# Performance work log

Hardware: AMD Instinct MI355X
Metric: run time of the kernel (lower is better)

Reference implementation:

```python
import jax, jax.numpy as jnp
import numpy as np

BS, C_IN, NY, NX = 8, 256, 80, 80
C, NC, NA, N = 256, 80, 1, 16384
K = 3  # 3x3 sparse convs, padding 1


def setup_inputs() -> dict:
    key = jax.random.key(0)
    ks = jax.random.split(key, 16)
    w = lambda k, shape: jax.random.normal(k, shape, jnp.float32) * 0.02
    x = jax.random.normal(ks[0], (BS, C_IN, NY, NX), jnp.float32)
    bi = jax.random.randint(ks[1], (N,), 0, BS)
    yi = jax.random.randint(ks[2], (N,), 0, NY)
    xi = jax.random.randint(ks[3], (N,), 0, NX)
    indices = jnp.stack([bi, yi, xi], axis=1).astype(jnp.int64)
    return {
        'x': x,
        'indices': indices,
        'stem_w': w(ks[4], (C, C_IN)),        'stem_b': w(ks[5], (C,)),
        'cls_conv_w': w(ks[6], (C, C * K * K)), 'cls_conv_b': w(ks[7], (C,)),
        'reg_conv_w': w(ks[8], (C, C * K * K)), 'reg_conv_b': w(ks[9], (C,)),
        'cls_pred_w': w(ks[10], (NA * NC, C)),  'cls_pred_b': w(ks[11], (NA * NC,)),
        'reg_pred_w': w(ks[12], (NA * 4, C)),   'reg_pred_b': w(ks[13], (NA * 4,)),
        'obj_pred_w': w(ks[14], (NA * 1, C)),   'obj_pred_b': w(ks[15], (NA * 1,)),
    }


def _gather_patches(stem, indices):
    """Gather flattened KxK patches at (b,y,x) indices.

    Matches F.unfold ordering: flattened as [c, kh, kw].
    stem: [bs, c, ny, nx] -> returns [N, c*K*K].
    """
    pad = K // 2
    # NHWC padded feature map: [bs, ny+2p, nx+2p, c]
    padded = jnp.pad(stem.transpose(0, 2, 3, 1),
                     ((0, 0), (pad, pad), (pad, pad), (0, 0)))
    bi, yi, xi = indices[:, 0], indices[:, 1], indices[:, 2]
    d = jnp.arange(K)
    yy = yi[:, None, None] + d[None, :, None]   # [N, K, 1]
    xx = xi[:, None, None] + d[None, None, :]   # [N, 1, K]
    patches = padded[bi[:, None, None], yy, xx]  # [N, K, K, c]
    n = patches.shape[0]
    return patches.transpose(0, 3, 1, 2).reshape(n, -1)  # [N, c*K*K]


def reference(x, indices, stem_w, stem_b, cls_conv_w, cls_conv_b,
              reg_conv_w, reg_conv_b, cls_pred_w, cls_pred_b,
              reg_pred_w, reg_pred_b, obj_pred_w, obj_pred_b):
    # dense 1x1 stem conv + SiLU
    stem = jax.nn.silu(jnp.einsum('bchw,oc->bohw', x, stem_w)
                       + stem_b[None, :, None, None])
    # sparse 3x3 convs: gather patches -> linear -> SiLU
    pf = _gather_patches(stem, indices)                 # [N, C*9]
    cls_feat = jax.nn.silu(pf @ cls_conv_w.T + cls_conv_b)
    reg_feat = jax.nn.silu(pf @ reg_conv_w.T + reg_conv_b)
    n = pf.shape[0]
    cls = (cls_feat @ cls_pred_w.T + cls_pred_b).reshape(n, NA, NC)
    reg = (reg_feat @ reg_pred_w.T + reg_pred_b).reshape(n, NA, 4)
    obj = (reg_feat @ obj_pred_w.T + obj_pred_b).reshape(n, NA, 1)
    y_sp = jnp.concatenate([reg, obj, cls], axis=-1).reshape(n, NA * (5 + NC))
    return y_sp
```

## Files before the change

### kernel.cpp

```cpp
#include <hip/hip_runtime.h>

typedef unsigned short u16;
typedef __attribute__((ext_vector_type(4))) float f32x4;
typedef __attribute__((ext_vector_type(8))) short s16x8;

#define BM 128
#define BN 128
#define BK 32

__device__ inline float bf2f(u16 u) {
    unsigned v = ((unsigned)u) << 16;
    return __builtin_bit_cast(float, v);
}
__device__ inline u16 f2bf(float f) {
    unsigned u = __builtin_bit_cast(unsigned, f);
    unsigned r = (u + 0x7FFFu + ((u >> 16) & 1u)) >> 16;
    return (u16)r;
}

typedef const __attribute__((address_space(1))) void* gptr_t;
typedef __attribute__((address_space(3))) void* lptr_t;
__device__ inline void gload16(const u16* gp, u16* lp) {
    __builtin_amdgcn_global_load_lds((gptr_t)gp, (lptr_t)lp, 16, 0, 0);
}

__global__ __launch_bounds__(256) void fused_pre(
    const float* __restrict__ x, const int* __restrict__ idx,
    const float* __restrict__ stem_w,
    const float* __restrict__ cls_conv_w, const float* __restrict__ cls_conv_b,
    const float* __restrict__ reg_conv_w, const float* __restrict__ reg_conv_b,
    const float* __restrict__ cls_pred_w, const float* __restrict__ cls_pred_b,
    const float* __restrict__ reg_pred_w, const float* __restrict__ reg_pred_b,
    const float* __restrict__ obj_pred_w, const float* __restrict__ obj_pred_b,
    u16* __restrict__ xT, u16* __restrict__ Wsb, u16* __restrict__ Wc,
    u16* __restrict__ Wf, int* __restrict__ rowoff,
    float* __restrict__ bc, float* __restrict__ bp, u16* __restrict__ zpage) {
    __shared__ u16 tile[64 * 258];
    const int blk = blockIdx.x;
    const int t = threadIdx.x;

    if (blk < 800) {
        int b = blk / 100, hw0 = (blk % 100) * 64;
        int l = t & 63, w = t >> 6;
        const float* xb = x + (size_t)b * 256 * 6400 + hw0 + l;
#pragma unroll 4
        for (int k = 0; k < 64; ++k) {
            int c = w + k * 4;
            tile[l * 258 + c] = f2bf(xb[(size_t)c * 6400]);
        }
        __syncthreads();
        u16* outb = xT + ((size_t)b * 6400 + hw0) * 256;
#pragma unroll
        for (int i = 0; i < 8; ++i) {
            int hw = w * 16 + i * 2 + (l >> 5);
            int c = (l & 31) * 8;
            *(int4*)(outb + (size_t)hw * 256 + c) = *(const int4*)&tile[hw * 258 + c];
        }
    } else if (blk < 1312) {
        int o = blk - 800;
        const float* src = (o < 256) ? (cls_conv_w + (size_t)o * 2304)
                                     : (reg_conv_w + (size_t)(o - 256) * 2304);
        u16* dst = Wc + (size_t)o * 2304;
#pragma unroll
        for (int it = 0; it < 9; ++it) {
            int kk = it * 256 + t;
            int j = kk >> 8, c = kk & 255;
            dst[kk] = f2bf(src[c * 9 + j]);
        }
    } else if (blk < 1888) {
        int i = (blk - 1312) * 256 + t;
        int n = i / 9, j = i % 9;
        int b = idx[n * 3 + 0], y = idx[n * 3 + 1], xx0 = idx[n * 3 + 2];
        int yy = y + j / 3 - 1;
        int xx = xx0 + j % 3 - 1;
        rowoff[i] = ((unsigned)yy < 80u && (unsigned)xx < 80u)
                        ? (b * 6400 + yy * 80 + xx) * 256 : -1;
    } else if (blk < 1952) {
        int base = (blk - 1888) * 1024;
#pragma unroll
        for (int it = 0; it < 4; ++it) {
            int i = base + it * 256 + t;
            Wsb[i] = f2bf(stem_w[i]);
        }
    } else if (blk < 1984) {
        int base = (blk - 1952) * 2048;
#pragma unroll
        for (int it = 0; it < 8; ++it) {
            int i = base + it * 256 + t;
            int o = i >> 9, k = i & 511;
            float v = 0.f;
            if (o < 4)       { if (k >= 256) v = reg_pred_w[o * 256 + (k - 256)]; }
            else if (o == 4) { if (k >= 256) v = obj_pred_w[k - 256]; }
            else if (o < 85) { if (k < 256)  v = cls_pred_w[(o - 5) * 256 + k]; }
            Wf[i] = f2bf(v);
        }
    } else {
        for (int i = t; i < 512; i += 256)
            bc[i] = (i < 256) ? cls_conv_b[i] : reg_conv_b[i - 256];
        if (t < 128) {
            float v = 0.f;
            if (t < 4) v = reg_pred_b[t];
            else if (t == 4) v = obj_pred_b[0];
            else if (t < 85) v = cls_pred_b[t - 5];
            bp[t] = v;
        }
        zpage[t] = 0;
    }
}

template <int EPI>
__global__ __launch_bounds__(256, 2) void gemm_bt(
    const u16* __restrict__ A, const u16* __restrict__ B,
    const float* __restrict__ bias, void* __restrict__ Dv,
    int K, int ldd, int storeN) {
    __shared__ __align__(16) u16 lA[BM * BK];
    __shared__ __align__(16) u16 lB[BN * BK];
    const int tid = threadIdx.x;
    const int lane = tid & 63;
    const int wid = tid >> 6;
    const int wm = wid >> 1, wn = wid & 1;
    const int m0 = blockIdx.x * BM;
    const int n0 = blockIdx.y * BN;

    const int srow = lane >> 2;
    const int scol = (lane & 3) * 8;
    const int arow = lane & 15;
    const int khalf = (lane >> 4) * 8;

    f32x4 acc[4][4] = {};

    for (int k0 = 0; k0 < K; k0 += BK) {
#pragma unroll
        for (int r = 0; r < 2; ++r) {
            int row = r * 64 + wid * 16 + srow;
            gload16(A + (size_t)(m0 + row) * K + k0 + scol, lA + r * 2048 + wid * 512);
            gload16(B + (size_t)(n0 + row) * K + k0 + scol, lB + r * 2048 + wid * 512);
        }
        __syncthreads();
        s16x8 af[4], bfr[4];
#pragma unroll
        for (int f = 0; f < 4; ++f) {
            af[f]  = *(const s16x8*)&lA[(wm * 64 + f * 16 + arow) * BK + khalf];
            bfr[f] = *(const s16x8*)&lB[(wn * 64 + f * 16 + arow) * BK + khalf];
        }
#pragma unroll
        for (int i = 0; i < 4; ++i)
#pragma unroll
            for (int j = 0; j < 4; ++j)
                acc[i][j] = __builtin_amdgcn_mfma_f32_16x16x32_bf16(af[i], bfr[j],
                                                                    acc[i][j], 0, 0, 0);
        __syncthreads();
    }

#pragma unroll
    for (int i = 0; i < 4; ++i) {
        int gr0 = m0 + wm * 64 + i * 16 + (lane >> 4) * 4;
#pragma unroll
        for (int j = 0; j < 4; ++j) {
            int gc = n0 + wn * 64 + j * 16 + (lane & 15);
            if (EPI == 1 && gc >= storeN) continue;
            float bb = bias[gc];
#pragma unroll
            for (int r = 0; r < 4; ++r) {
                float v = acc[i][j][r] + bb;
                if (EPI == 0) {
                    v = v / (1.0f + __expf(-v));
                    ((u16*)Dv)[(size_t)(gr0 + r) * ldd + gc] = f2bf(v);
                } else {
                    ((float*)Dv)[(size_t)(gr0 + r) * ldd + gc] = v;
                }
            }
        }
    }
}

__global__ __launch_bounds__(256, 4) void gemm_conv(
    const u16* __restrict__ stem, const int* __restrict__ rowoff,
    const u16* __restrict__ zpage, const u16* __restrict__ B,
    const float* __restrict__ bias, u16* __restrict__ D) {
    __shared__ __align__(16) u16 lA[128 * 64];
    __shared__ __align__(16) u16 lB[64 * 64];
    const int tid = threadIdx.x;
    const int lane = tid & 63;
    const int wid = tid >> 6;
    const int wm = wid >> 1, wn = wid & 1;
    const int m0 = blockIdx.x * 128;
    const int n0 = blockIdx.y * 64;

    const int srw = lane >> 3;
    const int cc  = lane & 7;
    const int arow = lane & 15;
    const int khi  = lane >> 4;

    f32x4 acc[4][2] = {};

    for (int k0 = 0; k0 < 2304; k0 += 64) {
        const int j  = k0 >> 8;
        const int c0 = k0 & 255;
        const int gch = (cc ^ srw) * 8;
#pragma unroll
        for (int r = 0; r < 4; ++r) {
            int row = r * 32 + wid * 8 + srw;
            int roff = rowoff[(m0 + row) * 9 + j];
            const u16* srcA = (roff < 0) ? (zpage + gch)
                                         : (stem + roff + c0 + gch);
            gload16(srcA, lA + (r * 32 + wid * 8) * 64);
        }
#pragma unroll
        for (int r = 0; r < 2; ++r) {
            int row = r * 32 + wid * 8 + srw;
            gload16(B + (size_t)(n0 + row) * 2304 + k0 + gch,
                    lB + (r * 32 + wid * 8) * 64);
        }
        __syncthreads();
        s16x8 af[2][4], bfr[2][2];
        const int sa = arow & 7;
#pragma unroll
        for (int f = 0; f < 4; ++f) {
            int ra = (wm * 64 + f * 16 + arow) * 64;
#pragma unroll
            for (int ks = 0; ks < 2; ++ks) {
                int q = ks * 4 + khi;
                af[ks][f] = *(const s16x8*)&lA[ra + ((q ^ sa) << 3)];
            }
        }
#pragma unroll
        for (int jj = 0; jj < 2; ++jj) {
            int rb = (wn * 32 + jj * 16 + arow) * 64;
#pragma unroll
            for (int ks = 0; ks < 2; ++ks) {
                int q = ks * 4 + khi;
                bfr[ks][jj] = *(const s16x8*)&lB[rb + ((q ^ sa) << 3)];
            }
        }
#pragma unroll
        for (int ks = 0; ks < 2; ++ks)
#pragma unroll
            for (int i = 0; i < 4; ++i)
#pragma unroll
                for (int jj = 0; jj < 2; ++jj)
                    acc[i][jj] = __builtin_amdgcn_mfma_f32_16x16x32_bf16(
                        af[ks][i], bfr[ks][jj], acc[i][jj], 0, 0, 0);
        __syncthreads();
    }

#pragma unroll
    for (int i = 0; i < 4; ++i) {
        int gr0 = m0 + wm * 64 + i * 16 + khi * 4;
#pragma unroll
        for (int jj = 0; jj < 2; ++jj) {
            int gc = n0 + wn * 32 + jj * 16 + arow;
            float bb = bias[gc];
#pragma unroll
            for (int r = 0; r < 4; ++r) {
                float v = acc[i][jj][r] + bb;
                v = v / (1.0f + __expf(-v));
                D[(size_t)(gr0 + r) * 512 + gc] = f2bf(v);
            }
        }
    }
}

__global__ __launch_bounds__(256, 4) void gemm_pred(
    const u16* __restrict__ A, const u16* __restrict__ B,
    const float* __restrict__ bias, float* __restrict__ D) {
    __shared__ __align__(16) u16 lA[64 * 64];
    __shared__ __align__(16) u16 lB[64 * 64];
    const int tid = threadIdx.x;
    const int lane = tid & 63;
    const int wid = tid >> 6;
    const int wm = wid >> 1, wn = wid & 1;
    const int m0 = blockIdx.x * 64;
    const int n0 = blockIdx.y * 64;

    const int srw = lane >> 3;
    const int cc  = lane & 7;
    const int arow = lane & 15;
    const int khi  = lane >> 4;

    f32x4 acc[2][2] = {};

    for (int k0 = 0; k0 < 512; k0 += 64) {
        const int gch = (cc ^ srw) * 8;
#pragma unroll
        for (int r = 0; r < 2; ++r) {
            int row = r * 32 + wid * 8 + srw;
            gload16(A + (size_t)(m0 + row) * 512 + k0 + gch,
                    lA + (r * 32 + wid * 8) * 64);
            gload16(B + (size_t)(n0 + row) * 512 + k0 + gch,
                    lB + (r * 32 + wid * 8) * 64);
        }
        __syncthreads();
        s16x8 af[2][2], bfr[2][2];
        const int sa = arow & 7;
#pragma unroll
        for (int f = 0; f < 2; ++f) {
            int ra = (wm * 32 + f * 16 + arow) * 64;
            int rb = (wn * 32 + f * 16 + arow) * 64;
#pragma unroll
            for (int ks = 0; ks < 2; ++ks) {
                int q = ks * 4 + khi;
                af[ks][f]  = *(const s16x8*)&lA[ra + ((q ^ sa) << 3)];
                bfr[ks][f] = *(const s16x8*)&lB[rb + ((q ^ sa) << 3)];
            }
        }
#pragma unroll
        for (int ks = 0; ks < 2; ++ks)
#pragma unroll
            for (int i = 0; i < 2; ++i)
#pragma unroll
                for (int jj = 0; jj < 2; ++jj)
                    acc[i][jj] = __builtin_amdgcn_mfma_f32_16x16x32_bf16(
                        af[ks][i], bfr[ks][jj], acc[i][jj], 0, 0, 0);
        __syncthreads();
    }

#pragma unroll
    for (int i = 0; i < 2; ++i) {
        int gr0 = m0 + wm * 32 + i * 16 + khi * 4;
#pragma unroll
        for (int jj = 0; jj < 2; ++jj) {
            int gc = n0 + wn * 32 + jj * 16 + arow;
            if (gc >= 85) continue;
            float bb = bias[gc];
#pragma unroll
            for (int r = 0; r < 4; ++r)
                D[(size_t)(gr0 + r) * 85 + gc] = acc[i][jj][r] + bb;
        }
    }
}

extern "C" void kernel_launch(void* const* d_in, const int* in_sizes, int n_in,
                              void* d_out, int out_size, void* d_ws, size_t ws_size,
                              hipStream_t stream) {
    const float* x          = (const float*)d_in[0];
    const int*   idx        = (const int*)d_in[1];
    const float* stem_w     = (const float*)d_in[2];
    const float* stem_b     = (const float*)d_in[3];
    const float* cls_conv_w = (const float*)d_in[4];
    const float* cls_conv_b = (const float*)d_in[5];
    const float* cls_pred_w = (const float*)d_in[8];
    const float* cls_pred_b = (const float*)d_in[9];
    const float* reg_conv_w = (const float*)d_in[6];
    const float* reg_conv_b = (const float*)d_in[7];
    const float* reg_pred_w = (const float*)d_in[10];
    const float* reg_pred_b = (const float*)d_in[11];
    const float* obj_pred_w = (const float*)d_in[12];
    const float* obj_pred_b = (const float*)d_in[13];
    float* out = (float*)d_out;
    char* ws = (char*)d_ws;

    u16*  xT     = (u16*)(ws);
    u16*  stem   = (u16*)(ws + 26214400);
    u16*  feat   = (u16*)(ws + 52428800);
    u16*  Wc     = (u16*)(ws + 69206016);
    u16*  Wf     = (u16*)(ws + 71565312);
    u16*  Wsb    = (u16*)(ws + 71696384);
    int*  rowoff = (int*)(ws + 71827456);
    u16*  zpage  = (u16*)(ws + 72417280);
    float* bc    = (float*)(ws + 72417792);
    float* bp    = (float*)(ws + 72419840);

    fused_pre<<<1985, 256, 0, stream>>>(x, idx, stem_w,
                                        cls_conv_w, cls_conv_b, reg_conv_w, reg_conv_b,
                                        cls_pred_w, cls_pred_b, reg_pred_w, reg_pred_b,
                                        obj_pred_w, obj_pred_b,
                                        xT, Wsb, Wc, Wf, rowoff, bc, bp, zpage);
    gemm_bt<0><<<dim3(400, 2), 256, 0, stream>>>(xT, Wsb, stem_b, stem, 256, 256, 256);
    gemm_conv<<<dim3(128, 8), 256, 0, stream>>>(stem, rowoff, zpage, Wc, bc, feat);
    gemm_pred<<<dim3(256, 2), 256, 0, stream>>>(feat, Wf, bp, out);
}
```

Before: 100.6 us.

## Triple-buffer LDS in gathered conv GEMM with async global-to-LDS prefetch

The gathered 3x3 conv GEMM now uses three LDS stages for A and B tiles. It issues global_load_lds for tile t+2 while computing tile t, and waits with explicit vmcnt counters plus a single barrier per tile in place of two syncthreads. The row-offset indices are prefetched a stage ahead, and the 36-step K loop is fully software-pipelined. This triples LDS use and lowers the launch-bounds occupancy hint from 4 to 2 blocks per CU, trading occupancy for latency hiding.

```diff
diff --git a/kernel.cpp b/kernel.cpp
--- a/kernel.cpp
+++ b/kernel.cpp
@@ -174,12 +174,12 @@
     }
 }
 
-__global__ __launch_bounds__(256, 4) void gemm_conv(
+__global__ __launch_bounds__(256, 2) void gemm_conv(
     const u16* __restrict__ stem, const int* __restrict__ rowoff,
     const u16* __restrict__ zpage, const u16* __restrict__ B,
     const float* __restrict__ bias, u16* __restrict__ D) {
-    __shared__ __align__(16) u16 lA[128 * 64];
-    __shared__ __align__(16) u16 lB[64 * 64];
+    __shared__ __align__(16) u16 lA[3][128 * 64];
+    __shared__ __align__(16) u16 lB[3][64 * 64];
     const int tid = threadIdx.x;
     const int lane = tid & 63;
     const int wid = tid >> 6;
@@ -189,60 +189,97 @@
 
     const int srw = lane >> 3;
     const int cc  = lane & 7;
+    const int gch = (cc ^ srw) * 8;
     const int arow = lane & 15;
     const int khi  = lane >> 4;
+    const int sa   = arow & 7;
 
     f32x4 acc[4][2] = {};
 
-    for (int k0 = 0; k0 < 2304; k0 += 64) {
-        const int j  = k0 >> 8;
-        const int c0 = k0 & 255;
-        const int gch = (cc ^ srw) * 8;
-#pragma unroll
-        for (int r = 0; r < 4; ++r) {
-            int row = r * 32 + wid * 8 + srw;
-            int roff = rowoff[(m0 + row) * 9 + j];
-            const u16* srcA = (roff < 0) ? (zpage + gch)
-                                         : (stem + roff + c0 + gch);
-            gload16(srcA, lA + (r * 32 + wid * 8) * 64);
-        }
-#pragma unroll
-        for (int r = 0; r < 2; ++r) {
-            int row = r * 32 + wid * 8 + srw;
-            gload16(B + (size_t)(n0 + row) * 2304 + k0 + gch,
-                    lB + (r * 32 + wid * 8) * 64);
-        }
-        __syncthreads();
-        s16x8 af[2][4], bfr[2][2];
-        const int sa = arow & 7;
-#pragma unroll
-        for (int f = 0; f < 4; ++f) {
-            int ra = (wm * 64 + f * 16 + arow) * 64;
-#pragma unroll
-            for (int ks = 0; ks < 2; ++ks) {
-                int q = ks * 4 + khi;
-                af[ks][f] = *(const s16x8*)&lA[ra + ((q ^ sa) << 3)];
-            }
-        }
-#pragma unroll
-        for (int jj = 0; jj < 2; ++jj) {
-            int rb = (wn * 32 + jj * 16 + arow) * 64;
-#pragma unroll
-            for (int ks = 0; ks < 2; ++ks) {
-                int q = ks * 4 + khi;
-                bfr[ks][jj] = *(const s16x8*)&lB[rb + ((q ^ sa) << 3)];
-            }
-        }
-#pragma unroll
-        for (int ks = 0; ks < 2; ++ks)
-#pragma unroll
-            for (int i = 0; i < 4; ++i)
-#pragma unroll
-                for (int jj = 0; jj < 2; ++jj)
-                    acc[i][jj] = __builtin_amdgcn_mfma_f32_16x16x32_bf16(
-                        af[ks][i], bfr[ks][jj], acc[i][jj], 0, 0, 0);
-        __syncthreads();
-    }
+    int rbase[4];
+#pragma unroll
+    for (int r = 0; r < 4; ++r) rbase[r] = (m0 + r * 32 + wid * 8 + srw) * 9;
+    const u16* Bp = B + (size_t)(n0 + wid * 8 + srw) * 2304 + gch;
+
+    int roP0[4], roP1[4];
+
+#define ROLOAD(ROP, JV)                                                         \
+    {   _Pragma("unroll")                                                       \
+        for (int r = 0; r < 4; ++r) ROP[r] = rowoff[rbase[r] + (JV)]; }
+
+#define STAGE(TS, BUF, ROP)                                                     \
+    {   const int c0_ = ((TS) & 3) << 6;                                        \
+        _Pragma("unroll")                                                       \
+        for (int r = 0; r < 4; ++r) {                                           \
+            int roff_ = ROP[r];                                                 \
+            const u16* sA_ = (roff_ < 0) ? (zpage + gch)                        \
+                                         : (stem + roff_ + c0_ + gch);          \
+            gload16(sA_, &lA[BUF][(r * 32 + wid * 8) * 64]);                    \
+        }                                                                       \
+        _Pragma("unroll")                                                       \
+        for (int r = 0; r < 2; ++r)                                             \
+            gload16(Bp + (size_t)(r * 32) * 2304 + (TS) * 64,                   \
+                    &lB[BUF][(r * 32 + wid * 8) * 64]); }
+
+#define COMPUTE(BUF)                                                            \
+    {   s16x8 af_[2][4], bf_[2][2];                                             \
+        _Pragma("unroll")                                                       \
+        for (int f = 0; f < 4; ++f) {                                           \
+            int ra_ = (wm * 64 + f * 16 + arow) * 64;                           \
+            _Pragma("unroll")                                                   \
+            for (int ks = 0; ks < 2; ++ks) {                                    \
+                int q_ = ks * 4 + khi;                                          \
+                af_[ks][f] = *(const s16x8*)&lA[BUF][ra_ + ((q_ ^ sa) << 3)];   \
+            }                                                                   \
+        }                                                                       \
+        _Pragma("unroll")                                                       \
+        for (int jj = 0; jj < 2; ++jj) {                                        \
+            int rb_ = (wn * 32 + jj * 16 + arow) * 64;                          \
+            _Pragma("unroll")                                                   \
+            for (int ks = 0; ks < 2; ++ks) {                                    \
+                int q_ = ks * 4 + khi;                                          \
+                bf_[ks][jj] = *(const s16x8*)&lB[BUF][rb_ + ((q_ ^ sa) << 3)];  \
+            }                                                                   \
+        }                                                                       \
+        _Pragma("unroll")                                                       \
+        for (int ks = 0; ks < 2; ++ks)                                          \
+            _Pragma("unroll")                                                   \
+            for (int i = 0; i < 4; ++i)                                         \
+                _Pragma("unroll")                                               \
+                for (int jj = 0; jj < 2; ++jj)                                  \
+                    acc[i][jj] = __builtin_amdgcn_mfma_f32_16x16x32_bf16(       \
+                        af_[ks][i], bf_[ks][jj], acc[i][jj], 0, 0, 0); }
+
+#define TILE_END(VM)                                                            \
+    {   asm volatile("s_waitcnt vmcnt(" #VM ")" ::: "memory");                  \
+        __builtin_amdgcn_s_barrier(); }
+
+    ROLOAD(roP0, 0);
+    ROLOAD(roP1, 0);
+    STAGE(0, 0, roP0);
+    STAGE(1, 1, roP1);
+    TILE_END(6);
+
+    for (int u = 0; u < 5; ++u) {
+        const int t0 = u * 6;
+        STAGE(t0 + 2, 2, roP0); ROLOAD(roP0, (t0 + 4) >> 2); COMPUTE(0); TILE_END(10);
+        STAGE(t0 + 3, 0, roP1); ROLOAD(roP1, (t0 + 5) >> 2); COMPUTE(1); TILE_END(10);
+        STAGE(t0 + 4, 1, roP0); ROLOAD(roP0, (t0 + 6) >> 2); COMPUTE(2); TILE_END(10);
+        STAGE(t0 + 5, 2, roP1); ROLOAD(roP1, (t0 + 7) >> 2); COMPUTE(0); TILE_END(10);
+        STAGE(t0 + 6, 0, roP0); ROLOAD(roP0, (t0 + 8) >> 2); COMPUTE(1); TILE_END(10);
+        STAGE(t0 + 7, 1, roP1); ROLOAD(roP1, (t0 + 9) >> 2); COMPUTE(2); TILE_END(10);
+    }
+    STAGE(32, 2, roP0); ROLOAD(roP0, 34 >> 2); COMPUTE(0); TILE_END(10);
+    STAGE(33, 0, roP1); ROLOAD(roP1, 35 >> 2); COMPUTE(1); TILE_END(10);
+    STAGE(34, 1, roP0);                        COMPUTE(2); TILE_END(6);
+    STAGE(35, 2, roP1);                        COMPUTE(0); TILE_END(6);
+                                               COMPUTE(1); TILE_END(0);
+                                               COMPUTE(2);
+
+#undef ROLOAD
+#undef STAGE
+#undef COMPUTE
+#undef TILE_END
 
 #pragma unroll
     for (int i = 0; i < 4; ++i) {
@@ -339,10 +376,10 @@
     const float* stem_b     = (const float*)d_in[3];
     const float* cls_conv_w = (const float*)d_in[4];
     const float* cls_conv_b = (const float*)d_in[5];
+    const float* reg_conv_w = (const float*)d_in[6];
+    const float* reg_conv_b = (const float*)d_in[7];
     const float* cls_pred_w = (const float*)d_in[8];
     const float* cls_pred_b = (const float*)d_in[9];
-    const float* reg_conv_w = (const float*)d_in[6];
-    const float* reg_conv_b = (const float*)d_in[7];
     const float* reg_pred_w = (const float*)d_in[10];
     const float* reg_pred_b = (const float*)d_in[11];
     const float* obj_pred_w = (const float*)d_in[12];
```

Result: slower. 107.9 us (+7.2%).
